# Kernel tuning notes

Measured on AMD Instinct MI355X. Metric: run time of the kernel, lower is better.

The kernel has to match this reference:

```python
import jax, jax.numpy as jnp
import numpy as np

N, E, B = 20000, 320000, 16
DIN, HID, HEADS, ZDIM = 128, 128, 4, 128
NEG_SLOPE = 0.2


def _glorot(key, shape):
    fan = sum(shape[-2:]) if len(shape) >= 2 else shape[-1] * 2
    return jax.random.normal(key, shape, jnp.float32) * jnp.sqrt(2.0 / fan)


def setup_inputs() -> dict:
    key = jax.random.key(0)
    ks = jax.random.split(key, 20)
    inp = {
        "x": jax.random.normal(ks[0], (N, DIN), jnp.float32),
        "edge_index": jax.random.randint(ks[1], (2, E), 0, N),
        "batch_id": jnp.sort(jax.random.randint(ks[2], (N,), 0, B)),
        "node_mask": jax.random.bernoulli(ks[3], 0.1, (N,)),
        "edge_mask": jax.random.bernoulli(ks[4], 0.5, (E,)),
    }
    # layer dims: e_Fs=[128,128,128,128]; heads=4 on layers 0,1; heads=1 last
    dims = [(DIN, HID, HEADS), (HID * HEADS, HID, HEADS), (HID * HEADS, ZDIM, 1)]
    for li, (fin, fout, h) in enumerate(dims, start=1):
        inp[f"W{li}"] = _glorot(ks[4 + 3 * li], (fin, h * fout))
        inp[f"att_src{li}"] = _glorot(ks[5 + 3 * li], (h, fout))
        inp[f"att_dst{li}"] = _glorot(ks[6 + 3 * li], (h, fout))
        inp[f"bias{li}"] = jnp.zeros((h * fout,), jnp.float32)
    return inp


def _gat_layer(x, W, a_src, a_dst, bias, src, dst, heads, fout):
    n = x.shape[0]
    h = (x @ W).reshape(n, heads, fout)            # [N,H,F]
    alpha_s = (h * a_src).sum(-1)                  # [N,H]
    alpha_d = (h * a_dst).sum(-1)                  # [N,H]
    e = jax.nn.leaky_relu(alpha_s[src] + alpha_d[dst], NEG_SLOPE)  # [E,H]
    m = jax.ops.segment_max(e, dst, num_segments=n)
    ex = jnp.exp(e - m[dst])
    denom = jax.ops.segment_sum(ex, dst, num_segments=n)
    w = ex / denom[dst]                            # segment softmax over incoming edges
    out = jax.ops.segment_sum(h[src] * w[:, :, None], dst, num_segments=n)  # [N,H,F]
    return out.reshape(n, heads * fout) + bias


def reference(x, edge_index, batch_id, node_mask, edge_mask,
              W1, att_src1, att_dst1, bias1,
              W2, att_src2, att_dst2, bias2,
              W3, att_src3, att_dst3, bias3):
    n = x.shape[0]
    loop = jnp.arange(n)
    src = jnp.concatenate([edge_index[0], loop])   # add_self_loops=True
    dst = jnp.concatenate([edge_index[1], loop])
    # edge_mask is passed as edge_attr but GATConv has edge_dim=None -> ignored
    h = _gat_layer(x, W1, att_src1, att_dst1, bias1, src, dst, HEADS, HID)
    h = jax.nn.relu(h)
    h = _gat_layer(h, W2, att_src2, att_dst2, bias2, src, dst, HEADS, HID)
    h = jax.nn.relu(h)
    h = _gat_layer(h, W3, att_src3, att_dst3, bias3, src, dst, 1, ZDIM)
    # masked global max pool: if mask.sum()>0 pool over ~mask else all nodes
    has_masked = jnp.any(node_mask)
    valid = jnp.logical_or(~node_mask, ~has_masked)
    neg = jnp.asarray(-1e30, h.dtype)
    vals = jnp.where(valid[:, None], h, neg)
    return jax.ops.segment_max(vals, batch_id, num_segments=B)
```

## Files before the change

kernel.cpp:

```cpp
#include <hip/hip_runtime.h>
#include <stdint.h>


#define NN 20000
#define MPAD 20096
#define NE 320000
#define NBATCH 16
#define NEG 0.2f
#define WSCALE 64.0f
#define WINV 0.015625f

using f16x8 = __attribute__((ext_vector_type(8))) _Float16;
using f32x4 = __attribute__((ext_vector_type(4))) float;

static __device__ __forceinline__ unsigned short h2u(_Float16 h) {
  union { _Float16 f; unsigned short u; } c;
  c.f = h;
  return c.u;
}
static __device__ __forceinline__ float f16lo(unsigned v) {
  union { unsigned short u; _Float16 f; } c;
  c.u = (unsigned short)(v & 0xFFFF);
  return (float)c.f;
}
static __device__ __forceinline__ float f16hi(unsigned v) {
  union { unsigned short u; _Float16 f; } c;
  c.u = (unsigned short)(v >> 16);
  return (float)c.f;
}
static __device__ __forceinline__ unsigned encf(float f) {
  unsigned u = __float_as_uint(f);
  return (u & 0x80000000u) ? ~u : (u | 0x80000000u);
}
static __device__ __forceinline__ float decf(unsigned u) {
  return __uint_as_float((u & 0x80000000u) ? (u ^ 0x80000000u) : ~u);
}

__global__ void k_init(int* deg, unsigned* enc) {
  int i = blockIdx.x * blockDim.x + threadIdx.x;
  if (i < NN) deg[i] = 1;
  if (i < NBATCH * 128) enc[i] = ~__float_as_uint(-1e30f);
}

__global__ void k_count(const int* __restrict__ ei, int* __restrict__ deg) {
  int e = blockIdx.x * blockDim.x + threadIdx.x;
  if (e < NE) atomicAdd(&deg[ei[NE + e]], 1);
}

__global__ void k_scan(const int* __restrict__ deg, int* __restrict__ row_ptr,
                       int* __restrict__ cursor) {
  __shared__ int wsum[16];
  int t = threadIdx.x;
  int lane = t & 63, wid = t >> 6;
  const int CH = 20;
  int beg = t * CH;
  int s = 0;
  for (int i = 0; i < CH; i++) {
    int idx = beg + i;
    if (idx < NN) s += deg[idx];
  }
  int incl = s;
  for (int off = 1; off < 64; off <<= 1) {
    int v = __shfl_up(incl, off, 64);
    if (lane >= off) incl += v;
  }
  if (lane == 63) wsum[wid] = incl;
  __syncthreads();
  if (t < 16) {
    int v = wsum[t];
    int in2 = v;
    for (int off = 1; off < 16; off <<= 1) {
      int u = __shfl_up(in2, off, 16);
      if (t >= off) in2 += u;
    }
    wsum[t] = in2 - v;
  }
  __syncthreads();
  int run = wsum[wid] + incl - s;
  for (int i = 0; i < CH; i++) {
    int idx = beg + i;
    if (idx < NN) {
      row_ptr[idx] = run;
      cursor[idx] = run;
      run += deg[idx];
    }
  }
  if (t == 1023) row_ptr[NN] = run;
}

__global__ void k_fill(const int* __restrict__ ei, int* __restrict__ cursor,
                       int* __restrict__ col, const int* __restrict__ nmask,
                       int* __restrict__ flag) {
  int i = blockIdx.x * blockDim.x + threadIdx.x;
  if (i >= NE + NN) return;
  int src, dst;
  if (i < NE) {
    src = ei[i];
    dst = ei[NE + i];
  } else {
    src = dst = i - NE;
    if (nmask[src] != 0) *flag = 1;
  }
  int pos = atomicAdd(&cursor[dst], 1);
  col[pos] = src;
}

__global__ void k_wprep(const float* __restrict__ W, unsigned short* __restrict__ wt,
                        int K, int Nc, int ncshift) {
  int idx = blockIdx.x * blockDim.x + threadIdx.x;
  int n = idx & (Nc - 1);
  int k = idx >> ncshift;
  float a = W[(size_t)k * Nc + n] * WSCALE;
  wt[(size_t)n * K + k] = h2u((_Float16)a);
}

__global__ void k_xsplit(const float* __restrict__ x, unsigned short* __restrict__ xp,
                         int total) {
  int idx = blockIdx.x * blockDim.x + threadIdx.x;
  if (idx >= total) return;
  xp[idx] = h2u((_Float16)x[idx]);
}

#define BM 128
#define BN 128
#define BK 32

__global__ __launch_bounds__(256, 3) void k_gemm(
    const unsigned short* __restrict__ Ap, const unsigned short* __restrict__ Wt,
    unsigned short* __restrict__ C, const float* __restrict__ attS,
    const float* __restrict__ attD, float* __restrict__ alS,
    float* __restrict__ alD, int K, int Nc, int H) {
  __shared__ __align__(16) unsigned short As[BM][BK];
  __shared__ __align__(16) unsigned short Bs[BN][BK];
  int tid = threadIdx.x;
  int bm = blockIdx.y * BM, bn = blockIdx.x * BN;
  int wid = tid >> 6, lane = tid & 63;
  int wm = (wid >> 1) * 64, wn = (wid & 1) * 64;
  int lrow = lane & 15, lquad = lane >> 4;

  f32x4 acc[4][4] = {};

  for (int k0 = 0; k0 < K; k0 += BK) {
    __syncthreads();
#pragma unroll
    for (int i = 0; i < 2; i++) {
      int slot = tid + 256 * i;
      int row = slot >> 2;
      int ks = (slot & 3) * 8;
      *(uint4*)&As[row][ks] = *(const uint4*)(Ap + (size_t)(bm + row) * K + k0 + ks);
      *(uint4*)&Bs[row][ks] = *(const uint4*)(Wt + (size_t)(bn + row) * K + k0 + ks);
    }
    __syncthreads();

    f16x8 af[4];
#pragma unroll
    for (int mf = 0; mf < 4; mf++)
      af[mf] = *(const f16x8*)&As[wm + mf * 16 + lrow][lquad * 8];
#pragma unroll
    for (int nf = 0; nf < 4; nf++) {
      f16x8 bf = *(const f16x8*)&Bs[wn + nf * 16 + lrow][lquad * 8];
#pragma unroll
      for (int mf = 0; mf < 4; mf++)
        acc[mf][nf] =
            __builtin_amdgcn_mfma_f32_16x16x32_f16(af[mf], bf, acc[mf][nf], 0, 0, 0);
    }
  }
#pragma unroll
  for (int mf = 0; mf < 4; mf++)
#pragma unroll
    for (int nf = 0; nf < 4; nf++)
#pragma unroll
      for (int r = 0; r < 4; r++) acc[mf][nf][r] *= WINV;
#pragma unroll
  for (int mf = 0; mf < 4; mf++) {
    int row0 = bm + wm + mf * 16 + lquad * 4;
#pragma unroll
    for (int nf = 0; nf < 4; nf++) {
      int colg = bn + wn + nf * 16 + lrow;
#pragma unroll
      for (int r = 0; r < 4; r++)
        C[(size_t)(row0 + r) * Nc + colg] = h2u((_Float16)acc[mf][nf][r]);
    }
  }
  float aSv[4], aDv[4];
#pragma unroll
  for (int nf = 0; nf < 4; nf++) {
    int colg = bn + wn + nf * 16 + lrow;
    aSv[nf] = attS[colg];
    aDv[nf] = attD[colg];
  }
  int head = bn >> 7;
#pragma unroll
  for (int mf = 0; mf < 4; mf++) {
#pragma unroll
    for (int r = 0; r < 4; r++) {
      float ps = 0.f, pd = 0.f;
#pragma unroll
      for (int nf = 0; nf < 4; nf++) {
        ps += acc[mf][nf][r] * aSv[nf];
        pd += acc[mf][nf][r] * aDv[nf];
      }
#pragma unroll
      for (int off = 1; off < 16; off <<= 1) {
        ps += __shfl_xor(ps, off, 64);
        pd += __shfl_xor(pd, off, 64);
      }
      int row = bm + wm + mf * 16 + lquad * 4 + r;
      if (lrow == 0) {
        atomicAdd(&alS[(size_t)row * H + head], ps);
        atomicAdd(&alD[(size_t)row * H + head], pd);
      }
    }
  }
}

template <int H, int WPN, bool RELU, bool FP16OUT>
__global__ __launch_bounds__(256) void k_agg(
    const unsigned short* __restrict__ h, const float* __restrict__ as_,
    const float* __restrict__ ad_, const int* __restrict__ row_ptr,
    const int* __restrict__ col, const float* __restrict__ bias,
    float* __restrict__ out, unsigned short* __restrict__ outp) {
  constexpr int HF = H * 128, FPW = HF / WPN, PL = FPW / 64, HH = H / WPN;
  __shared__ float el[4][HH][64];
  __shared__ float wl[4][HH][64];
  __shared__ int cl[4][64];
  int tid = threadIdx.x, bwid = tid >> 6, lane = tid & 63;
  int gwid = blockIdx.x * 4 + bwid;
  int node = gwid / WPN, sub = gwid - node * WPN;
  if (node >= NN) return;
  const int hb = sub * HH;
  int beg = row_ptr[node], end = row_ptr[node + 1];
  int deg = end - beg;

  float adv[HH], m[HH], s[HH];
#pragma unroll
  for (int i = 0; i < HH; i++) {
    adv[i] = ad_[(size_t)node * H + hb + i];
    m[i] = -1e30f;
    s[i] = 0.f;
  }
  for (int j = beg + lane; j < end; j += 64) {
    int sidx = col[j];
    cl[bwid][lane] = sidx;
#pragma unroll
    for (int i = 0; i < HH; i++) {
      float e = as_[(size_t)sidx * H + hb + i] + adv[i];
      e = (e > 0.f) ? e : NEG * e;
      el[bwid][i][lane] = e;
      float nm = fmaxf(m[i], e);
      s[i] = s[i] * __expf(m[i] - nm) + __expf(e - nm);
      m[i] = nm;
    }
  }
  float Mr[HH], Sinv[HH];
#pragma unroll
  for (int i = 0; i < HH; i++) {
    float mm = m[i];
#pragma unroll
    for (int off = 32; off; off >>= 1) mm = fmaxf(mm, __shfl_xor(mm, off, 64));
    float t = s[i] * __expf(m[i] - mm);
#pragma unroll
    for (int off = 32; off; off >>= 1) t += __shfl_xor(t, off, 64);
    Mr[i] = mm;
    Sinv[i] = 1.f / t;
  }
  const int fbase = sub * FPW + lane * PL;
  const int ih = (lane * PL) >> 7;
  float acc[PL] = {};
  for (int c0 = beg; c0 < end; c0 += 64) {
    int cnt = min(64, end - c0);
    if (deg <= 64) {
      if (lane < cnt) {
#pragma unroll
        for (int i = 0; i < HH; i++)
          wl[bwid][i][lane] = __expf(el[bwid][i][lane] - Mr[i]) * Sinv[i];
      }
    } else {
      if (lane < cnt) {
        int sidx = col[c0 + lane];
        cl[bwid][lane] = sidx;
#pragma unroll
        for (int i = 0; i < HH; i++) {
          float e = as_[(size_t)sidx * H + hb + i] + adv[i];
          e = (e > 0.f) ? e : NEG * e;
          wl[bwid][i][lane] = __expf(e - Mr[i]) * Sinv[i];
        }
      }
    }
    for (int je = 0; je < cnt; je += 8) {
      float wv[8];
      int sv[8];
#pragma unroll
      for (int r = 0; r < 8; r++) {
        int ok = (je + r) < cnt;
        int idx = ok ? (je + r) : 0;
        sv[r] = cl[bwid][idx];
        wv[r] = ok ? wl[bwid][ih][idx] : 0.f;
      }
      if constexpr (PL == 4) {
        uint2 v[8];
#pragma unroll
        for (int r = 0; r < 8; r++)
          v[r] = *(const uint2*)(h + (size_t)sv[r] * HF + fbase);
#pragma unroll
        for (int r = 0; r < 8; r++) {
          acc[0] += wv[r] * f16lo(v[r].x);
          acc[1] += wv[r] * f16hi(v[r].x);
          acc[2] += wv[r] * f16lo(v[r].y);
          acc[3] += wv[r] * f16hi(v[r].y);
        }
      } else {
        unsigned v[8];
#pragma unroll
        for (int r = 0; r < 8; r++)
          v[r] = *(const unsigned*)(h + (size_t)sv[r] * HF + fbase);
#pragma unroll
        for (int r = 0; r < 8; r++) {
          acc[0] += wv[r] * f16lo(v[r]);
          acc[1] += wv[r] * f16hi(v[r]);
        }
      }
    }
  }
  float vv[PL];
#pragma unroll
  for (int i = 0; i < PL; i++) {
    float v = acc[i] + bias[fbase + i];
    if (RELU) v = fmaxf(v, 0.f);
    vv[i] = v;
  }
  if constexpr (FP16OUT) {
    if constexpr (PL == 4) {
      ushort4 o;
      o.x = h2u((_Float16)vv[0]);
      o.y = h2u((_Float16)vv[1]);
      o.z = h2u((_Float16)vv[2]);
      o.w = h2u((_Float16)vv[3]);
      *(ushort4*)(outp + (size_t)node * HF + fbase) = o;
    } else {
      ushort2 o;
      o.x = h2u((_Float16)vv[0]);
      o.y = h2u((_Float16)vv[1]);
      *(ushort2*)(outp + (size_t)node * HF + fbase) = o;
    }
  } else {
    float* op = out + (size_t)node * HF + fbase;
#pragma unroll
    for (int i = 0; i < PL; i++) op[i] = vv[i];
  }
}

__global__ void k_pool(const float* __restrict__ h, const int* __restrict__ batch,
                       const int* __restrict__ mask, const int* __restrict__ flag,
                       unsigned* __restrict__ enc) {
  int f = threadIdx.x;
  int n0 = blockIdx.x * 32;
  if (n0 >= NN) return;
  int n1 = min(NN, n0 + 32);
  int any = *flag;
  float local = -1e30f;
  int curb = batch[n0];
  for (int n = n0; n < n1; ++n) {
    int b = batch[n];
    if (b != curb) {
      if (local > -1e30f) atomicMax(&enc[curb * 128 + f], encf(local));
      local = -1e30f;
      curb = b;
    }
    bool valid = (mask[n] == 0) || (!any);
    if (valid) local = fmaxf(local, h[(size_t)n * 128 + f]);
  }
  if (local > -1e30f) atomicMax(&enc[curb * 128 + f], encf(local));
}

__global__ void k_out(const unsigned* __restrict__ enc, float* __restrict__ out) {
  int i = blockIdx.x * blockDim.x + threadIdx.x;
  if (i < NBATCH * 128) out[i] = decf(enc[i]);
}

extern "C" void kernel_launch(void* const* d_in, const int* in_sizes, int n_in,
                              void* d_out, int out_size, void* d_ws, size_t ws_size,
                              hipStream_t stream) {
  const float* x = (const float*)d_in[0];
  const int* ei = (const int*)d_in[1];
  const int* batch = (const int*)d_in[2];
  const int* nmask = (const int*)d_in[3];
  const float* W1 = (const float*)d_in[5];
  const float* as1 = (const float*)d_in[6];
  const float* ad1 = (const float*)d_in[7];
  const float* b1 = (const float*)d_in[8];
  const float* W2 = (const float*)d_in[9];
  const float* as2 = (const float*)d_in[10];
  const float* ad2 = (const float*)d_in[11];
  const float* b2 = (const float*)d_in[12];
  const float* W3 = (const float*)d_in[13];
  const float* as3 = (const float*)d_in[14];
  const float* ad3 = (const float*)d_in[15];
  const float* b3 = (const float*)d_in[16];

  char* ws = (char*)d_ws;
  size_t off = 0;
  auto alloc = [&](size_t bytes) -> char* {
    char* p = ws + off;
    off = (off + bytes + 255) & ~(size_t)255;
    return p;
  };
  unsigned short* hA = (unsigned short*)alloc((size_t)MPAD * 512 * 2);
  unsigned short* hG = (unsigned short*)alloc((size_t)MPAD * 512 * 2);
  float* out3 = (float*)alloc((size_t)MPAD * 128 * 4);
  unsigned short* xP = (unsigned short*)out3;
  unsigned short* wt1 = (unsigned short*)alloc((size_t)512 * 128 * 2);
  unsigned short* wt2 = (unsigned short*)alloc((size_t)512 * 512 * 2);
  unsigned short* wt3 = (unsigned short*)alloc((size_t)128 * 512 * 2);
  char* alStart = ws + off;
  float* alS1 = (float*)alloc((size_t)MPAD * 4 * 4);
  float* alD1 = (float*)alloc((size_t)MPAD * 4 * 4);
  float* alS2 = (float*)alloc((size_t)MPAD * 4 * 4);
  float* alD2 = (float*)alloc((size_t)MPAD * 4 * 4);
  float* alS3 = (float*)alloc((size_t)MPAD * 4);
  float* alD3 = (float*)alloc((size_t)MPAD * 4);
  size_t alBytes = (size_t)((ws + off) - alStart);
  int* deg = (int*)alloc((size_t)NN * 4);
  int* cursor = (int*)alloc((size_t)NN * 4);
  int* rowp = (int*)alloc((size_t)(NN + 1) * 4);
  int* colx = (int*)alloc((size_t)(NE + NN) * 4);
  unsigned* enc = (unsigned*)alloc((size_t)NBATCH * 128 * 4);
  int* flag = (int*)alloc(4);
  (void)ws_size; (void)n_in; (void)in_sizes; (void)out_size;

  hipMemsetAsync(flag, 0, 4, stream);
  hipMemsetAsync(alStart, 0, alBytes, stream);
  k_init<<<(NN + 255) / 256, 256, 0, stream>>>(deg, enc);
  k_count<<<(NE + 255) / 256, 256, 0, stream>>>(ei, deg);
  k_scan<<<1, 1024, 0, stream>>>(deg, rowp, cursor);
  k_fill<<<(NE + NN + 255) / 256, 256, 0, stream>>>(ei, cursor, colx, nmask, flag);

  k_wprep<<<(512 * 128) / 256, 256, 0, stream>>>(W1, wt1, 128, 512, 9);
  k_wprep<<<(512 * 512) / 256, 256, 0, stream>>>(W2, wt2, 512, 512, 9);
  k_wprep<<<(128 * 512) / 256, 256, 0, stream>>>(W3, wt3, 512, 128, 7);
  k_xsplit<<<(NN * 128 + 255) / 256, 256, 0, stream>>>(x, xP, NN * 128);

  dim3 gg1(512 / BN, MPAD / BM);
  dim3 gg3(1, MPAD / BM);

  k_gemm<<<gg1, 256, 0, stream>>>(xP, wt1, hA, as1, ad1, alS1, alD1, 128, 512, 4);
  k_agg<4, 2, true, true><<<(NN * 2 + 3) / 4, 256, 0, stream>>>(
      hA, alS1, alD1, rowp, colx, b1, nullptr, hG);
  k_gemm<<<gg1, 256, 0, stream>>>(hG, wt2, hA, as2, ad2, alS2, alD2, 512, 512, 4);
  k_agg<4, 2, true, true><<<(NN * 2 + 3) / 4, 256, 0, stream>>>(
      hA, alS2, alD2, rowp, colx, b2, nullptr, hG);
  k_gemm<<<gg3, 256, 0, stream>>>(hG, wt3, hA, as3, ad3, alS3, alD3, 512, 128, 1);
  k_agg<1, 1, false, false><<<(NN + 3) / 4, 256, 0, stream>>>(
      hA, alS3, alD3, rowp, colx, b3, out3, nullptr);

  k_pool<<<(NN + 31) / 32, 128, 0, stream>>>(out3, batch, nmask, flag, enc);
  k_out<<<(NBATCH * 128 + 255) / 256, 256, 0, stream>>>(enc, (float*)d_out);
}
```

Before: 386.2 us.

## Merge init and prep kernels, transpose MFMA operands for vectorized GEMM epilogue

Replaces the two memsets plus init kernel with one init kernel that also zeroes the alpha buffers and the flag. The three weight-prep kernels and the x conversion are fused into a single launch. In the GEMM the MFMA operands are swapped, so each lane holds four consecutive output columns for one row. That lets the epilogue write ushort4 stores, load float4 attention vectors, and reduce alpha with two shuffles instead of four. The aims are fewer launches and cheaper epilogue stores and reductions; the layout change must stay consistent with how C is indexed.

```diff
diff --git a/kernel.cpp b/kernel.cpp
--- a/kernel.cpp
+++ b/kernel.cpp
@@ -36,10 +36,12 @@
   return __uint_as_float((u & 0x80000000u) ? (u ^ 0x80000000u) : ~u);
 }
 
-__global__ void k_init(int* deg, unsigned* enc) {
+__global__ void k_init0(int* deg, unsigned* enc, int* flag, float* alz, int alcount) {
   int i = blockIdx.x * blockDim.x + threadIdx.x;
   if (i < NN) deg[i] = 1;
   if (i < NBATCH * 128) enc[i] = ~__float_as_uint(-1e30f);
+  if (i == 0) *flag = 0;
+  for (int j = i; j < alcount; j += gridDim.x * blockDim.x) alz[j] = 0.f;
 }
 
 __global__ void k_count(const int* __restrict__ ei, int* __restrict__ deg) {
@@ -105,20 +107,31 @@
   col[pos] = src;
 }
 
-__global__ void k_wprep(const float* __restrict__ W, unsigned short* __restrict__ wt,
-                        int K, int Nc, int ncshift) {
+#define R1 (512 * 128)
+#define R2 (512 * 512)
+#define R3 (128 * 512)
+__global__ void k_prep(const float* __restrict__ W1, const float* __restrict__ W2,
+                       const float* __restrict__ W3, const float* __restrict__ x,
+                       unsigned short* __restrict__ wt1,
+                       unsigned short* __restrict__ wt2,
+                       unsigned short* __restrict__ wt3,
+                       unsigned short* __restrict__ xp) {
   int idx = blockIdx.x * blockDim.x + threadIdx.x;
-  int n = idx & (Nc - 1);
-  int k = idx >> ncshift;
-  float a = W[(size_t)k * Nc + n] * WSCALE;
-  wt[(size_t)n * K + k] = h2u((_Float16)a);
-}
-
-__global__ void k_xsplit(const float* __restrict__ x, unsigned short* __restrict__ xp,
-                         int total) {
-  int idx = blockIdx.x * blockDim.x + threadIdx.x;
-  if (idx >= total) return;
-  xp[idx] = h2u((_Float16)x[idx]);
+  if (idx < R1) {
+    int n = idx & 511, k = idx >> 9;
+    wt1[(size_t)n * 128 + k] = h2u((_Float16)(W1[(size_t)k * 512 + n] * WSCALE));
+  } else if (idx < R1 + R2) {
+    int j = idx - R1;
+    int n = j & 511, k = j >> 9;
+    wt2[(size_t)n * 512 + k] = h2u((_Float16)(W2[(size_t)k * 512 + n] * WSCALE));
+  } else if (idx < R1 + R2 + R3) {
+    int j = idx - (R1 + R2);
+    int n = j & 127, k = j >> 7;
+    wt3[(size_t)n * 512 + k] = h2u((_Float16)(W3[(size_t)k * 128 + n] * WSCALE));
+  } else {
+    int j = idx - (R1 + R2 + R3);
+    if (j < NN * 128) xp[j] = h2u((_Float16)x[j]);
+  }
 }
 
 #define BM 128
@@ -162,7 +175,7 @@
 #pragma unroll
       for (int mf = 0; mf < 4; mf++)
         acc[mf][nf] =
-            __builtin_amdgcn_mfma_f32_16x16x32_f16(af[mf], bf, acc[mf][nf], 0, 0, 0);
+            __builtin_amdgcn_mfma_f32_16x16x32_f16(bf, af[mf], acc[mf][nf], 0, 0, 0);
     }
   }
 #pragma unroll
@@ -171,45 +184,47 @@
     for (int nf = 0; nf < 4; nf++)
 #pragma unroll
       for (int r = 0; r < 4; r++) acc[mf][nf][r] *= WINV;
+
+  float4 aS[4], aD[4];
+#pragma unroll
+  for (int nf = 0; nf < 4; nf++) {
+    int n0 = bn + wn + nf * 16 + lquad * 4;
+    aS[nf] = *(const float4*)(attS + n0);
+    aD[nf] = *(const float4*)(attD + n0);
+  }
+  int head = bn >> 7;
 #pragma unroll
   for (int mf = 0; mf < 4; mf++) {
-    int row0 = bm + wm + mf * 16 + lquad * 4;
+    float ps = 0.f, pd = 0.f;
 #pragma unroll
     for (int nf = 0; nf < 4; nf++) {
-      int colg = bn + wn + nf * 16 + lrow;
-#pragma unroll
-      for (int r = 0; r < 4; r++)
-        C[(size_t)(row0 + r) * Nc + colg] = h2u((_Float16)acc[mf][nf][r]);
-    }
-  }
-  float aSv[4], aDv[4];
-#pragma unroll
-  for (int nf = 0; nf < 4; nf++) {
-    int colg = bn + wn + nf * 16 + lrow;
-    aSv[nf] = attS[colg];
-    aDv[nf] = attD[colg];
-  }
-  int head = bn >> 7;
+      ps += acc[mf][nf][0] * aS[nf].x + acc[mf][nf][1] * aS[nf].y +
+            acc[mf][nf][2] * aS[nf].z + acc[mf][nf][3] * aS[nf].w;
+      pd += acc[mf][nf][0] * aD[nf].x + acc[mf][nf][1] * aD[nf].y +
+            acc[mf][nf][2] * aD[nf].z + acc[mf][nf][3] * aD[nf].w;
+    }
+    ps += __shfl_xor(ps, 16, 64);
+    ps += __shfl_xor(ps, 32, 64);
+    pd += __shfl_xor(pd, 16, 64);
+    pd += __shfl_xor(pd, 32, 64);
+    int row = bm + wm + mf * 16 + lrow;
+    if (lquad == 0) {
+      atomicAdd(&alS[(size_t)row * H + head], ps);
+      atomicAdd(&alD[(size_t)row * H + head], pd);
+    }
+  }
 #pragma unroll
   for (int mf = 0; mf < 4; mf++) {
-#pragma unroll
-    for (int r = 0; r < 4; r++) {
-      float ps = 0.f, pd = 0.f;
-#pragma unroll
-      for (int nf = 0; nf < 4; nf++) {
-        ps += acc[mf][nf][r] * aSv[nf];
-        pd += acc[mf][nf][r] * aDv[nf];
-      }
-#pragma unroll
-      for (int off = 1; off < 16; off <<= 1) {
-        ps += __shfl_xor(ps, off, 64);
-        pd += __shfl_xor(pd, off, 64);
-      }
-      int row = bm + wm + mf * 16 + lquad * 4 + r;
-      if (lrow == 0) {
-        atomicAdd(&alS[(size_t)row * H + head], ps);
-        atomicAdd(&alD[(size_t)row * H + head], pd);
-      }
+    int m = bm + wm + mf * 16 + lrow;
+#pragma unroll
+    for (int nf = 0; nf < 4; nf++) {
+      int n0 = bn + wn + nf * 16 + lquad * 4;
+      ushort4 o;
+      o.x = h2u((_Float16)acc[mf][nf][0]);
+      o.y = h2u((_Float16)acc[mf][nf][1]);
+      o.z = h2u((_Float16)acc[mf][nf][2]);
+      o.w = h2u((_Float16)acc[mf][nf][3]);
+      *(ushort4*)(C + (size_t)m * Nc + n0) = o;
     }
   }
 }
@@ -419,7 +434,7 @@
   float* alD2 = (float*)alloc((size_t)MPAD * 4 * 4);
   float* alS3 = (float*)alloc((size_t)MPAD * 4);
   float* alD3 = (float*)alloc((size_t)MPAD * 4);
-  size_t alBytes = (size_t)((ws + off) - alStart);
+  int alcount = (int)(((ws + off) - alStart) / 4);
   int* deg = (int*)alloc((size_t)NN * 4);
   int* cursor = (int*)alloc((size_t)NN * 4);
   int* rowp = (int*)alloc((size_t)(NN + 1) * 4);
@@ -428,17 +443,15 @@
   int* flag = (int*)alloc(4);
   (void)ws_size; (void)n_in; (void)in_sizes; (void)out_size;
 
-  hipMemsetAsync(flag, 0, 4, stream);
-  hipMemsetAsync(alStart, 0, alBytes, stream);
-  k_init<<<(NN + 255) / 256, 256, 0, stream>>>(deg, enc);
+  k_init0<<<(alcount + 255) / 256, 256, 0, stream>>>((int*)deg, enc, flag,
+                                                     (float*)alStart, alcount);
   k_count<<<(NE + 255) / 256, 256, 0, stream>>>(ei, deg);
   k_scan<<<1, 1024, 0, stream>>>(deg, rowp, cursor);
   k_fill<<<(NE + NN + 255) / 256, 256, 0, stream>>>(ei, cursor, colx, nmask, flag);
-
-  k_wprep<<<(512 * 128) / 256, 256, 0, stream>>>(W1, wt1, 128, 512, 9);
-  k_wprep<<<(512 * 512) / 256, 256, 0, stream>>>(W2, wt2, 512, 512, 9);
-  k_wprep<<<(128 * 512) / 256, 256, 0, stream>>>(W3, wt3, 512, 128, 7);
-  k_xsplit<<<(NN * 128 + 255) / 256, 256, 0, stream>>>(x, xP, NN * 128);
+  {
+    int total = R1 + R2 + R3 + NN * 128;
+    k_prep<<<(total + 255) / 256, 256, 0, stream>>>(W1, W2, W3, x, wt1, wt2, wt3, xP);
+  }
 
   dim3 gg1(512 / BN, MPAD / BM);
   dim3 gg3(1, MPAD / BM);
```

Result: faster. 356.3 us (-7.7%).
